# Performance work log

Hardware: AMD Instinct MI355X
Metric: run time of the kernel (lower is better)

Reference implementation:

```python
import jax, jax.numpy as jnp
import numpy as np

V, E, H = 32000, 256, 512  # vocab, embedding_size, hidden_size
B, T = 64, 512             # batch, seq_len


def setup_inputs() -> dict:
    key = jax.random.key(0)
    ks = jax.random.split(key, 8)
    inputs = jax.random.randint(ks[0], (B, T), 0, V)
    lengths = jax.random.randint(ks[1], (B,), 0, T)
    reset_indices = jax.random.randint(ks[2], (B, T), 0, 2, dtype=jnp.int32)
    # nn.Embedding: N(0,1) init with padding_idx row zeroed
    emb = jax.random.normal(ks[3], (V, E), dtype=jnp.float32).at[0].set(0.0)
    # nn.LSTMCell params: uniform(-1/sqrt(H), 1/sqrt(H)), gate order i,f,g,o
    s = 1.0 / np.sqrt(H)
    W_ih = jax.random.uniform(ks[4], (4 * H, E), minval=-s, maxval=s, dtype=jnp.float32)
    W_hh = jax.random.uniform(ks[5], (4 * H, H), minval=-s, maxval=s, dtype=jnp.float32)
    b_ih = jax.random.uniform(ks[6], (4 * H,), minval=-s, maxval=s, dtype=jnp.float32)
    b_hh = jax.random.uniform(ks[7], (4 * H,), minval=-s, maxval=s, dtype=jnp.float32)
    return {"inputs": inputs, "lengths": lengths, "reset_indices": reset_indices,
            "emb": emb, "W_ih": W_ih, "W_hh": W_hh, "b_ih": b_ih, "b_hh": b_hh}


def reference(inputs, lengths, reset_indices, emb, W_ih, W_hh, b_ih, b_hh):
    x = emb[inputs]                                        # (B,T,E); dropout is identity in eval
    mask = (jnp.arange(T) < lengths[:, None]).astype(x.dtype)   # (B,T) length mask
    xt = jnp.swapaxes(x, 0, 1)                             # (T,B,E) time-major
    m_t = mask.T                                           # (T,B)
    r_t = reset_indices.astype(x.dtype).T                  # (T,B)
    # precompute input contribution to gates for all timesteps
    gates_x = jnp.einsum('tbe,ge->tbg', xt, W_ih) + b_ih + b_hh  # (T,B,4H)

    def step(carry, inp):
        h, c = carry
        gx, m, r = inp
        g = gx + h @ W_hh.T                                # (B,4H)
        i, f, gg, o = jnp.split(g, 4, axis=-1)
        i = jax.nn.sigmoid(i); f = jax.nn.sigmoid(f)
        gg = jnp.tanh(gg); o = jax.nn.sigmoid(o)
        c_new = f * c + i * gg
        h_new = o * jnp.tanh(c_new)
        mm = m[:, None]; rr = r[:, None]
        h_next = h_new * mm + h * (1 - mm)                 # mask-blend (keep state past length)
        c_next = c_new * mm + c * (1 - mm)
        # reset zeroing applied to carried state AFTER output is recorded
        return (h_next * (1 - rr), c_next * (1 - rr)), h_next

    h0 = jnp.zeros((B, H), dtype=x.dtype)
    (hT, cT), out_t = jax.lax.scan(step, (h0, h0), (gates_x, m_t, r_t))  # out_t: (T,B,H)
    output = jnp.swapaxes(out_t, 0, 1)                     # (B,T,H) = output.transpose(0,1)
    return output, hT, cT, mask
```

## Files before the change

kernel.cpp:

```cpp
#include <hip/hip_runtime.h>
#include <stdint.h>
#include <stddef.h>

constexpr int V = 32000, E = 256, H = 512, B = 64, T = 512;
constexpr int NTHR = 512;
constexpr int NBLK = 64;
constexpr int BATG = 16;
constexpr int HPB = 32;

constexpr int PSW = 128 * 17;
constexpr int OFF_PS   = 0;
constexpr int OFF_BIAS = OFF_PS + 8 * PSW * 4;
constexpr int OFF_LEN  = OFF_BIAS + 128 * 4;
constexpr int LDS_BYTES = 84 * 1024;

constexpr size_t OUT_HT   = (size_t)B * T * H;
constexpr size_t OUT_CT   = OUT_HT + (size_t)B * H;
constexpr size_t OUT_MASK = OUT_CT + (size_t)B * H;

typedef __attribute__((ext_vector_type(8))) short short8;
typedef __attribute__((ext_vector_type(4))) float f32x4;
typedef __attribute__((ext_vector_type(4))) unsigned int u32x4;

__device__ __forceinline__ unsigned short f2bf(float f) {
  uint32_t u = __builtin_bit_cast(uint32_t, f);
  return (unsigned short)((u + 0x7fffu + ((u >> 16) & 1u)) >> 16);
}
__device__ __forceinline__ short8 pack_bf8(float4 v0, float4 v1) {
  short8 r;
  r[0] = (short)f2bf(v0.x); r[1] = (short)f2bf(v0.y);
  r[2] = (short)f2bf(v0.z); r[3] = (short)f2bf(v0.w);
  r[4] = (short)f2bf(v1.x); r[5] = (short)f2bf(v1.y);
  r[6] = (short)f2bf(v1.z); r[7] = (short)f2bf(v1.w);
  return r;
}
__device__ __forceinline__ float sigmoidf_fast(float x) {
  return 1.f / (1.f + __expf(-x));
}
__device__ __forceinline__ float tanhf_fast(float x) {
  return 1.f - 2.f / (__expf(2.f * x) + 1.f);
}
__device__ __forceinline__ void st_word(uint32_t* p, uint32_t v) {
  __hip_atomic_store(p, v, __ATOMIC_RELAXED, __HIP_MEMORY_SCOPE_AGENT);
}
__device__ __forceinline__ void ld_mall_4x4(const uint32_t* p, u32x4& r0,
                                            u32x4& r1, u32x4& r2, u32x4& r3) {
  asm volatile(
      "global_load_dwordx4 %0, %4, off sc1\n\t"
      "global_load_dwordx4 %1, %4, off offset:64 sc1\n\t"
      "global_load_dwordx4 %2, %4, off offset:128 sc1\n\t"
      "global_load_dwordx4 %3, %4, off offset:192 sc1\n\t"
      "s_waitcnt vmcnt(0)"
      : "=&v"(r0), "=&v"(r1), "=&v"(r2), "=&v"(r3)
      : "v"(p)
      : "memory");
}

__global__ void __launch_bounds__(NTHR, 1)
lstm_mfma(const int* __restrict__ inputs, const int* __restrict__ lengths,
          const int* __restrict__ resets, const float* __restrict__ emb,
          const float* __restrict__ W_ih, const float* __restrict__ W_hh,
          const float* __restrict__ b_ih, const float* __restrict__ b_hh,
          float* __restrict__ out, int* __restrict__ ctr,
          uint32_t* __restrict__ hw) {
  extern __shared__ char lds[];
  float* Ps = (float*)(lds + OFF_PS);
  float* Bias = (float*)(lds + OFF_BIAS);
  int* Lens = (int*)(lds + OFF_LEN);

  const int tid = threadIdx.x;
  const int blk = blockIdx.x;
  const int grp = blk & 3;
  const int rq = blk >> 2;
  const int khid = rq * HPB;
  const int b0 = grp * BATG;
  int* flags = ctr + grp * 64;

  const int w = tid >> 6;
  const int L = tid & 63;
  const int lc = L & 15;
  const int q = L >> 4;

  short8 wf[4][8];
  if (w < 4) {
    #pragma unroll
    for (int s = 0; s < 4; ++s) {
      #pragma unroll
      for (int tl = 0; tl < 8; ++tl) {
        const int n = 16 * tl + lc;
        const int grow = (n >> 5) * H + khid + (n & 31);
        const float* src = W_hh + (size_t)grow * H + 128 * w + 32 * s + 8 * q;
        wf[s][tl] = pack_bf8(*(const float4*)src, *(const float4*)(src + 4));
      }
    }
  } else {
    #pragma unroll
    for (int s = 0; s < 2; ++s) {
      #pragma unroll
      for (int tl = 0; tl < 8; ++tl) {
        const int n = 16 * tl + lc;
        const int grow = (n >> 5) * H + khid + (n & 31);
        const float* src = W_ih + (size_t)grow * E + 64 * (w - 4) + 32 * s + 8 * q;
        wf[s][tl] = pack_bf8(*(const float4*)src, *(const float4*)(src + 4));
      }
    }
  }
  if (tid < 128) {
    const int grow = (tid >> 5) * H + khid + (tid & 31);
    Bias[tid] = b_ih[grow] + b_hh[grow];
  }
  if (tid < 16) Lens[tid] = lengths[b0 + tid];
  {
    int i = blk * 512 + tid;
    int mb = i >> 9, mt = i & (T - 1);
    out[OUT_MASK + i] = (mt < lengths[mb]) ? 1.f : 0.f;
  }
  __syncthreads();

  const int jj = tid & 31;
  const int bb = tid >> 5;

  float carry_h = 0.f, carry_c = 0.f;

  for (int t = 0; t < T; ++t) {
    const uint32_t* hsrc = hw + (size_t)(t & 1) * (B * 256);
    uint32_t* hdst = hw + (size_t)((t + 1) & 1) * (B * 256);

    float rr = (float)resets[(b0 + bb) * T + t];
    f32x4 acc[8];
    #pragma unroll
    for (int tl = 0; tl < 8; ++tl) acc[tl] = (f32x4){0.f, 0.f, 0.f, 0.f};

    if (w >= 4) {
      const int tok = inputs[(b0 + lc) * T + t];
      const float* eb = emb + (size_t)tok * E + 64 * (w - 4) + 8 * q;
      short8 a0 = pack_bf8(*(const float4*)eb, *(const float4*)(eb + 4));
      short8 a1 = pack_bf8(*(const float4*)(eb + 32), *(const float4*)(eb + 36));
      #pragma unroll
      for (int tl = 0; tl < 8; ++tl)
        acc[tl] = __builtin_amdgcn_mfma_f32_16x16x32_bf16(a0, wf[0][tl], acc[tl], 0, 0, 0);
      #pragma unroll
      for (int tl = 0; tl < 8; ++tl)
        acc[tl] = __builtin_amdgcn_mfma_f32_16x16x32_bf16(a1, wf[1][tl], acc[tl], 0, 0, 0);
    }

    if (t > 0) {
      if (w == 0) {
        for (;;) {
          int v = 0x7fffffff;
          if (L < 16) v = __hip_atomic_load(&flags[L], __ATOMIC_RELAXED,
                                            __HIP_MEMORY_SCOPE_AGENT);
          if (__all(v >= t)) break;
          __builtin_amdgcn_s_sleep(1);
        }
      }
      __syncthreads();
      if (w < 4) {
        const uint32_t* p = hsrc + (size_t)(b0 + lc) * 256 + 64 * w + 4 * q;
        u32x4 r0, r1, r2, r3;
        ld_mall_4x4(p, r0, r1, r2, r3);
        short8 a0 = __builtin_bit_cast(short8, r0);
        short8 a1 = __builtin_bit_cast(short8, r1);
        short8 a2 = __builtin_bit_cast(short8, r2);
        short8 a3 = __builtin_bit_cast(short8, r3);
        #pragma unroll
        for (int tl = 0; tl < 8; ++tl)
          acc[tl] = __builtin_amdgcn_mfma_f32_16x16x32_bf16(a0, wf[0][tl], acc[tl], 0, 0, 0);
        #pragma unroll
        for (int tl = 0; tl < 8; ++tl)
          acc[tl] = __builtin_amdgcn_mfma_f32_16x16x32_bf16(a1, wf[1][tl], acc[tl], 0, 0, 0);
        #pragma unroll
        for (int tl = 0; tl < 8; ++tl)
          acc[tl] = __builtin_amdgcn_mfma_f32_16x16x32_bf16(a2, wf[2][tl], acc[tl], 0, 0, 0);
        #pragma unroll
        for (int tl = 0; tl < 8; ++tl)
          acc[tl] = __builtin_amdgcn_mfma_f32_16x16x32_bf16(a3, wf[3][tl], acc[tl], 0, 0, 0);
      }
    }

    #pragma unroll
    for (int tl = 0; tl < 8; ++tl)
      *(f32x4*)(Ps + w * PSW + (16 * tl + lc) * 17 + 4 * q) = acc[tl];
    __syncthreads();

    float g4[4];
    #pragma unroll
    for (int gi = 0; gi < 4; ++gi) {
      const int n = gi * 32 + jj;
      float s = Bias[n];
      #pragma unroll
      for (int ww = 0; ww < 8; ++ww) s += Ps[ww * PSW + n * 17 + bb];
      g4[gi] = s;
    }
    float ig = sigmoidf_fast(g4[0]);
    float fg = sigmoidf_fast(g4[1]);
    float gg = tanhf_fast(g4[2]);
    float og = sigmoidf_fast(g4[3]);
    float c_new = fg * carry_c + ig * gg;
    float h_new = og * tanhf_fast(c_new);
    bool live = (t < Lens[bb]);
    float h_next = live ? h_new : carry_h;
    float c_next = live ? c_new : carry_c;
    carry_h = h_next * (1.f - rr);
    carry_c = c_next * (1.f - rr);

    float ph = __shfl(carry_h, L ^ 1);
    if (t < T - 1) {
      if ((tid & 1) == 0) {
        uint32_t word = (uint32_t)f2bf(carry_h) | ((uint32_t)f2bf(ph) << 16);
        st_word(hdst + (size_t)(b0 + bb) * 256 + 16 * rq + (jj >> 1), word);
      }
      __syncthreads();
      if (tid == 0)
        __hip_atomic_store(&flags[rq], t + 1, __ATOMIC_RELAXED,
                           __HIP_MEMORY_SCOPE_AGENT);
    }
    out[((size_t)(b0 + bb) * T + t) * H + khid + jj] = h_next;
  }
  out[OUT_HT + (size_t)(b0 + bb) * H + khid + jj] = carry_h;
  out[OUT_CT + (size_t)(b0 + bb) * H + khid + jj] = carry_c;
}

extern "C" void kernel_launch(void* const* d_in, const int* in_sizes, int n_in,
                              void* d_out, int out_size, void* d_ws, size_t ws_size,
                              hipStream_t stream) {
  const int* inputs    = (const int*)d_in[0];
  const int* lengths   = (const int*)d_in[1];
  const int* resets    = (const int*)d_in[2];
  const float* emb     = (const float*)d_in[3];
  const float* W_ih    = (const float*)d_in[4];
  const float* W_hh    = (const float*)d_in[5];
  const float* b_ih    = (const float*)d_in[6];
  const float* b_hh    = (const float*)d_in[7];
  float* out = (float*)d_out;

  int* ctr = (int*)d_ws;
  uint32_t* hw = (uint32_t*)((char*)d_ws + 4096);

  hipFuncSetAttribute((const void*)lstm_mfma,
                      hipFuncAttributeMaxDynamicSharedMemorySize, LDS_BYTES);

  hipMemsetAsync(d_ws, 0, 4096, stream);
  lstm_mfma<<<NBLK, NTHR, LDS_BYTES, stream>>>(
      inputs, lengths, resets, emb, W_ih, W_hh, b_ih, b_hh, out, ctr, hw);
}
```

Baseline: 2.056 ms.

## Replace flag-based inter-block sync with timestep-tagged hidden-state words

Each hidden value is now stored as a 32-bit word holding the bf16 value in the low half and the step number in the high half. Consumer waves spin directly on the data until every tag matches the expected step, which removes the separate flag array, the flag store and one block barrier per step. The partial-sum LDS buffer is double-buffered so that the post-store barrier can be dropped. In exchange, each step reads twice as many bytes of hidden state and relies on each 32-bit store being observed atomically. The workspace is no longer zeroed, so correctness depends on stale tags never matching the expected step.

Result: slower. 2.673 ms (+30.0%).

```diff
diff --git a/kernel.cpp b/kernel.cpp
--- a/kernel.cpp
+++ b/kernel.cpp
@@ -10,9 +10,11 @@
 
 constexpr int PSW = 128 * 17;
 constexpr int OFF_PS   = 0;
-constexpr int OFF_BIAS = OFF_PS + 8 * PSW * 4;
+constexpr int OFF_BIAS = OFF_PS + 2 * 8 * PSW * 4;
 constexpr int OFF_LEN  = OFF_BIAS + 128 * 4;
-constexpr int LDS_BYTES = 84 * 1024;
+constexpr int LDS_BYTES = OFF_LEN + 64;
+
+constexpr int BHW = B * 512;
 
 constexpr size_t OUT_HT   = (size_t)B * T * H;
 constexpr size_t OUT_CT   = OUT_HT + (size_t)B * H;
@@ -43,15 +45,21 @@
 __device__ __forceinline__ void st_word(uint32_t* p, uint32_t v) {
   __hip_atomic_store(p, v, __ATOMIC_RELAXED, __HIP_MEMORY_SCOPE_AGENT);
 }
-__device__ __forceinline__ void ld_mall_4x4(const uint32_t* p, u32x4& r0,
-                                            u32x4& r1, u32x4& r2, u32x4& r3) {
+__device__ __forceinline__ void ld_tagged_8x4(const uint32_t* p,
+    u32x4& r0, u32x4& r1, u32x4& r2, u32x4& r3,
+    u32x4& r4, u32x4& r5, u32x4& r6, u32x4& r7) {
   asm volatile(
-      "global_load_dwordx4 %0, %4, off sc1\n\t"
-      "global_load_dwordx4 %1, %4, off offset:64 sc1\n\t"
-      "global_load_dwordx4 %2, %4, off offset:128 sc1\n\t"
-      "global_load_dwordx4 %3, %4, off offset:192 sc1\n\t"
+      "global_load_dwordx4 %0, %8, off sc1\n\t"
+      "global_load_dwordx4 %1, %8, off offset:16 sc1\n\t"
+      "global_load_dwordx4 %2, %8, off offset:128 sc1\n\t"
+      "global_load_dwordx4 %3, %8, off offset:144 sc1\n\t"
+      "global_load_dwordx4 %4, %8, off offset:256 sc1\n\t"
+      "global_load_dwordx4 %5, %8, off offset:272 sc1\n\t"
+      "global_load_dwordx4 %6, %8, off offset:384 sc1\n\t"
+      "global_load_dwordx4 %7, %8, off offset:400 sc1\n\t"
       "s_waitcnt vmcnt(0)"
-      : "=&v"(r0), "=&v"(r1), "=&v"(r2), "=&v"(r3)
+      : "=&v"(r0), "=&v"(r1), "=&v"(r2), "=&v"(r3),
+        "=&v"(r4), "=&v"(r5), "=&v"(r6), "=&v"(r7)
       : "v"(p)
       : "memory");
 }
@@ -61,8 +69,7 @@
           const int* __restrict__ resets, const float* __restrict__ emb,
           const float* __restrict__ W_ih, const float* __restrict__ W_hh,
           const float* __restrict__ b_ih, const float* __restrict__ b_hh,
-          float* __restrict__ out, int* __restrict__ ctr,
-          uint32_t* __restrict__ hw) {
+          float* __restrict__ out, uint32_t* __restrict__ hw) {
   extern __shared__ char lds[];
   float* Ps = (float*)(lds + OFF_PS);
   float* Bias = (float*)(lds + OFF_BIAS);
@@ -74,7 +81,6 @@
   const int rq = blk >> 2;
   const int khid = rq * HPB;
   const int b0 = grp * BATG;
-  int* flags = ctr + grp * 64;
 
   const int w = tid >> 6;
   const int L = tid & 63;
@@ -115,7 +121,6 @@
     int mb = i >> 9, mt = i & (T - 1);
     out[OUT_MASK + i] = (mt < lengths[mb]) ? 1.f : 0.f;
   }
-  __syncthreads();
 
   const int jj = tid & 31;
   const int bb = tid >> 5;
@@ -123,8 +128,7 @@
   float carry_h = 0.f, carry_c = 0.f;
 
   for (int t = 0; t < T; ++t) {
-    const uint32_t* hsrc = hw + (size_t)(t & 1) * (B * 256);
-    uint32_t* hdst = hw + (size_t)((t + 1) & 1) * (B * 256);
+    float* Pcur = Ps + (t & 1) * (8 * PSW);
 
     float rr = (float)resets[(b0 + bb) * T + t];
     f32x4 acc[8];
@@ -142,45 +146,46 @@
       #pragma unroll
       for (int tl = 0; tl < 8; ++tl)
         acc[tl] = __builtin_amdgcn_mfma_f32_16x16x32_bf16(a1, wf[1][tl], acc[tl], 0, 0, 0);
-    }
-
-    if (t > 0) {
-      if (w == 0) {
-        for (;;) {
-          int v = 0x7fffffff;
-          if (L < 16) v = __hip_atomic_load(&flags[L], __ATOMIC_RELAXED,
-                                            __HIP_MEMORY_SCOPE_AGENT);
-          if (__all(v >= t)) break;
-          __builtin_amdgcn_s_sleep(1);
+    } else if (t > 0) {
+      const uint32_t* p = hw + (size_t)(t & 1) * BHW +
+                          (size_t)(b0 + lc) * 512 + 128 * w + 8 * q;
+      const uint32_t expt = (uint32_t)t << 16;
+      u32x4 r0, r1, r2, r3, r4, r5, r6, r7;
+      for (;;) {
+        ld_tagged_8x4(p, r0, r1, r2, r3, r4, r5, r6, r7);
+        uint32_t d = 0;
+        #pragma unroll
+        for (int j = 0; j < 4; ++j) {
+          d |= (r0[j] ^ expt) & 0xffff0000u;
+          d |= (r1[j] ^ expt) & 0xffff0000u;
+          d |= (r2[j] ^ expt) & 0xffff0000u;
+          d |= (r3[j] ^ expt) & 0xffff0000u;
+          d |= (r4[j] ^ expt) & 0xffff0000u;
+          d |= (r5[j] ^ expt) & 0xffff0000u;
+          d |= (r6[j] ^ expt) & 0xffff0000u;
+          d |= (r7[j] ^ expt) & 0xffff0000u;
         }
-      }
-      __syncthreads();
-      if (w < 4) {
-        const uint32_t* p = hsrc + (size_t)(b0 + lc) * 256 + 64 * w + 4 * q;
-        u32x4 r0, r1, r2, r3;
-        ld_mall_4x4(p, r0, r1, r2, r3);
-        short8 a0 = __builtin_bit_cast(short8, r0);
-        short8 a1 = __builtin_bit_cast(short8, r1);
-        short8 a2 = __builtin_bit_cast(short8, r2);
-        short8 a3 = __builtin_bit_cast(short8, r3);
+        if (__all(d == 0)) break;
+        __builtin_amdgcn_s_sleep(1);
+      }
+      u32x4 rl[8] = {r0, r1, r2, r3, r4, r5, r6, r7};
+      #pragma unroll
+      for (int s = 0; s < 4; ++s) {
+        short8 a;
+        #pragma unroll
+        for (int j = 0; j < 4; ++j) {
+          a[j]     = (short)(rl[2 * s][j] & 0xffffu);
+          a[4 + j] = (short)(rl[2 * s + 1][j] & 0xffffu);
+        }
         #pragma unroll
         for (int tl = 0; tl < 8; ++tl)
-          acc[tl] = __builtin_amdgcn_mfma_f32_16x16x32_bf16(a0, wf[0][tl], acc[tl], 0, 0, 0);
-        #pragma unroll
-        for (int tl = 0; tl < 8; ++tl)
-          acc[tl] = __builtin_amdgcn_mfma_f32_16x16x32_bf16(a1, wf[1][tl], acc[tl], 0, 0, 0);
-        #pragma unroll
-        for (int tl = 0; tl < 8; ++tl)
-          acc[tl] = __builtin_amdgcn_mfma_f32_16x16x32_bf16(a2, wf[2][tl], acc[tl], 0, 0, 0);
-        #pragma unroll
-        for (int tl = 0; tl < 8; ++tl)
-          acc[tl] = __builtin_amdgcn_mfma_f32_16x16x32_bf16(a3, wf[3][tl], acc[tl], 0, 0, 0);
+          acc[tl] = __builtin_amdgcn_mfma_f32_16x16x32_bf16(a, wf[s][tl], acc[tl], 0, 0, 0);
       }
     }
 
     #pragma unroll
     for (int tl = 0; tl < 8; ++tl)
-      *(f32x4*)(Ps + w * PSW + (16 * tl + lc) * 17 + 4 * q) = acc[tl];
+      *(f32x4*)(Pcur + w * PSW + (16 * tl + lc) * 17 + 4 * q) = acc[tl];
     __syncthreads();
 
     float g4[4];
@@ -189,7 +194,7 @@
       const int n = gi * 32 + jj;
       float s = Bias[n];
       #pragma unroll
-      for (int ww = 0; ww < 8; ++ww) s += Ps[ww * PSW + n * 17 + bb];
+      for (int ww = 0; ww < 8; ++ww) s += Pcur[ww * PSW + n * 17 + bb];
       g4[gi] = s;
     }
     float ig = sigmoidf_fast(g4[0]);
@@ -204,16 +209,10 @@
     carry_h = h_next * (1.f - rr);
     carry_c = c_next * (1.f - rr);
 
-    float ph = __shfl(carry_h, L ^ 1);
     if (t < T - 1) {
-      if ((tid & 1) == 0) {
-        uint32_t word = (uint32_t)f2bf(carry_h) | ((uint32_t)f2bf(ph) << 16);
-        st_word(hdst + (size_t)(b0 + bb) * 256 + 16 * rq + (jj >> 1), word);
-      }
-      __syncthreads();
-      if (tid == 0)
-        __hip_atomic_store(&flags[rq], t + 1, __ATOMIC_RELAXED,
-                           __HIP_MEMORY_SCOPE_AGENT);
+      uint32_t word = ((uint32_t)(t + 1) << 16) | (uint32_t)f2bf(carry_h);
+      st_word(hw + (size_t)((t + 1) & 1) * BHW +
+                  (size_t)(b0 + bb) * 512 + 32 * rq + jj, word);
     }
     out[((size_t)(b0 + bb) * T + t) * H + khid + jj] = h_next;
   }
@@ -234,13 +233,11 @@
   const float* b_hh    = (const float*)d_in[7];
   float* out = (float*)d_out;
 
-  int* ctr = (int*)d_ws;
-  uint32_t* hw = (uint32_t*)((char*)d_ws + 4096);
+  uint32_t* hw = (uint32_t*)d_ws;
 
   hipFuncSetAttribute((const void*)lstm_mfma,
                       hipFuncAttributeMaxDynamicSharedMemorySize, LDS_BYTES);
 
-  hipMemsetAsync(d_ws, 0, 4096, stream);
   lstm_mfma<<<NBLK, NTHR, LDS_BYTES, stream>>>(
-      inputs, lengths, resets, emb, W_ih, W_hh, b_ih, b_hh, out, ctr, hw);
-}
+      inputs, lengths, resets, emb, W_ih, W_hh, b_ih, b_hh, out, hw);
+}
```
